# Kernel optimization log

Measured on AMD Instinct MI355X. Metric: run time of the kernel, lower is better.

Reference implementation:

```python
import jax, jax.numpy as jnp
import numpy as np

RANK = 4
ALPHA = 4.0
SCALE = ALPHA / RANK


def setup_inputs() -> dict:
    key = jax.random.key(0)
    k1, k2, k3, k4 = jax.random.split(key, 4)
    B, S, H = 4, 2048, 2048
    NH, HD = 16, 128
    x = jax.random.normal(k1, (B, S, H), dtype=jnp.float32)
    W_orig = jax.random.normal(k2, (H, NH, HD), dtype=jnp.float32) * (1.0 / np.sqrt(H))
    A_kernel = jax.random.normal(k3, (H, RANK), dtype=jnp.float32) * (1.0 / RANK)
    # B kernel is zero-init in the module; use small randn so the LoRA path is exercised
    B_kernel = jax.random.normal(k4, (RANK, NH, HD), dtype=jnp.float32) * 0.02
    return {"x": x, "W_orig": W_orig, "A_kernel": A_kernel, "B_kernel": B_kernel}


def reference(x, W_orig, A_kernel, B_kernel):
    # original layer: EinsumDense 'abc,cde->abde'  [B,S,H] x [H,NH,HD] -> [B,S,NH,HD]
    original_output = jnp.einsum('bsc,chd->bshd', x, W_orig)
    # LoRA path: Dense to rank, then EinsumDense back up, scaled
    ax = x @ A_kernel                                   # [B,S,r]
    lora_output = jnp.einsum('bsr,rhd->bshd', ax, B_kernel) * SCALE
    return original_output + lora_output
```

## Files before the change

kernel.cpp:

```cpp
#include <hip/hip_runtime.h>
#include <hip/hip_bf16.h>
#include <cstdint>


using bf16 = __hip_bfloat16;
typedef __attribute__((ext_vector_type(8))) __bf16 bf16x8;
typedef __attribute__((ext_vector_type(4))) float f32x4;

constexpr int Mdim = 8192;
constexpr int Ndim = 2048;
constexpr int Kdim = 2048;
constexpr float SCALE = 1.0f;

constexpr int BM = 256, BN = 256, BK = 64;
constexpr int NT2 = Kdim / (2 * BK);
constexpr int CVT_BLOCKS = (Mdim * Kdim) / (256 * 8);
constexpr int PREP_BLOCKS = (Ndim / 64) * (Kdim / 64);

__device__ __forceinline__ void gload_lds16(const void* g, void* l) {
  __builtin_amdgcn_global_load_lds(
      (const __attribute__((address_space(1))) uint32_t*)g,
      (__attribute__((address_space(3))) uint32_t*)l,
      16, 0, 0);
}

__global__ void prep_all(const float* __restrict__ X,
                         const float* __restrict__ W,
                         const float* __restrict__ A,
                         const float* __restrict__ Bk,
                         uint16_t* __restrict__ Xb,
                         uint16_t* __restrict__ Wt) {
  __shared__ float tile[64][65];

  if (blockIdx.x < CVT_BLOCKS) {
    const int i = blockIdx.x * blockDim.x + threadIdx.x;
    const float4* Xv = (const float4*)X;
    float4 a = Xv[i * 2 + 0];
    float4 b = Xv[i * 2 + 1];
    uint16_t o[8];
    o[0] = __bfloat16_as_ushort(__float2bfloat16(a.x));
    o[1] = __bfloat16_as_ushort(__float2bfloat16(a.y));
    o[2] = __bfloat16_as_ushort(__float2bfloat16(a.z));
    o[3] = __bfloat16_as_ushort(__float2bfloat16(a.w));
    o[4] = __bfloat16_as_ushort(__float2bfloat16(b.x));
    o[5] = __bfloat16_as_ushort(__float2bfloat16(b.y));
    o[6] = __bfloat16_as_ushort(__float2bfloat16(b.z));
    o[7] = __bfloat16_as_ushort(__float2bfloat16(b.w));
    *reinterpret_cast<uint4*>(Xb + (size_t)i * 8) = *reinterpret_cast<uint4*>(o);
  } else {
    const int pid = blockIdx.x - CVT_BLOCKS;
    const int tx = threadIdx.x & 63;
    const int ty = threadIdx.x >> 6;
    const int n0 = (pid & 31) * 64, k0 = (pid >> 5) * 64;

    const int n = n0 + tx;
    const float b0 = Bk[0 * Ndim + n];
    const float b1 = Bk[1 * Ndim + n];
    const float b2 = Bk[2 * Ndim + n];
    const float b3 = Bk[3 * Ndim + n];

    for (int i = ty; i < 64; i += 4) {
      const int k = k0 + i;
      float w = W[(size_t)k * Ndim + n];
      w += SCALE * (A[k * 4 + 0] * b0 + A[k * 4 + 1] * b1 +
                    A[k * 4 + 2] * b2 + A[k * 4 + 3] * b3);
      tile[tx][i] = w;
    }
    __syncthreads();
    for (int i = ty; i < 64; i += 4) {
      Wt[(size_t)(n0 + i) * Kdim + (k0 + tx)] =
          __bfloat16_as_ushort(__float2bfloat16(tile[i][tx]));
    }
  }
}

#define FENCE() asm volatile("" ::: "memory")
#define VMW(N)  asm volatile("s_waitcnt vmcnt(" #N ")" ::: "memory")
#define LGKM8() asm volatile("s_waitcnt lgkmcnt(8)" ::: "memory")
#define PMID()                                                                 \
  do {                                                                         \
    FENCE();                                                                   \
    __builtin_amdgcn_s_barrier();                                              \
    asm volatile("s_waitcnt lgkmcnt(0)" ::: "memory");                         \
  } while (0)
#define PEND()                                                                 \
  do {                                                                         \
    FENCE();                                                                   \
    __builtin_amdgcn_s_barrier();                                              \
    FENCE();                                                                   \
  } while (0)

__global__ __launch_bounds__(512, 2) void gemm_8ph(
    const uint16_t* __restrict__ X, const uint16_t* __restrict__ Wt,
    float* __restrict__ out) {
  __shared__ uint16_t lds[65536];

  const int t = threadIdx.x;
  const int wave = t >> 6, lane = t & 63;
  const int wm = wave >> 2, wn = wave & 3;
  const int l15 = lane & 15, kg = lane >> 4;
  const int sw = l15 & 7;

  const int lid = blockIdx.x;
  const int xcd = lid & 7, loc = lid >> 3;
  const int by = xcd * 4 + (loc & 3);
  const int bx = loc >> 2;
  const int m0 = by * BM, n0 = bx * BN;

  const uint16_t* Ag = X + (size_t)m0 * Kdim;
  const uint16_t* Bg = Wt + (size_t)n0 * Kdim;

  const int r8 = lane >> 3;
  const int gc = (lane & 7) ^ r8;
  const int slot0 = wave * 2, slot1 = slot0 + 1;
  const size_t go0 = (size_t)(slot0 * 8 + r8) * Kdim + gc * 8;
  const size_t go1 = (size_t)(slot1 * 8 + r8) * Kdim + gc * 8;

  int aE[2], bE[2];
#pragma unroll
  for (int s2 = 0; s2 < 2; ++s2) {
    const int p = (s2 * 4 + kg) ^ sw;
    aE[s2] = (wm * 64 + l15) * 64 + p * 8;
    bE[s2] = (wn * 32 + l15) * 64 + p * 8;
  }

#define STAGE_A(buf, h, kt)                                                    \
  do {                                                                         \
    gload_lds16(Ag + go0 + (size_t)(h) * 128 * Kdim + (kt),                    \
                &lds[(buf) * 32768 + (h) * 8192 + slot0 * 512]);               \
    gload_lds16(Ag + go1 + (size_t)(h) * 128 * Kdim + (kt),                    \
                &lds[(buf) * 32768 + (h) * 8192 + slot1 * 512]);               \
  } while (0)
#define STAGE_B(buf, h, kt)                                                    \
  do {                                                                         \
    gload_lds16(Bg + go0 + (size_t)(h) * 128 * Kdim + (kt),                    \
                &lds[(buf) * 32768 + 16384 + (h) * 8192 + slot0 * 512]);       \
    gload_lds16(Bg + go1 + (size_t)(h) * 128 * Kdim + (kt),                    \
                &lds[(buf) * 32768 + 16384 + (h) * 8192 + slot1 * 512]);       \
  } while (0)

  bf16x8 a[4][2], b0[2][2], b1[2][2];
  f32x4 acc[8][4] = {};

#define READ_A(QM, buf)                                                        \
  do {                                                                         \
    _Pragma("unroll") for (int ii = 0; ii < 4; ++ii)                           \
        _Pragma("unroll") for (int s2 = 0; s2 < 2; ++s2)                       \
            a[ii][s2] = *reinterpret_cast<const bf16x8*>(                      \
                &lds[(buf) * 32768 + (QM) * 8192 + ii * 1024 + aE[s2]]);       \
  } while (0)
#define READ_B(QN, buf, dst)                                                   \
  do {                                                                         \
    _Pragma("unroll") for (int jj = 0; jj < 2; ++jj)                           \
        _Pragma("unroll") for (int s2 = 0; s2 < 2; ++s2)                       \
            dst[jj][s2] = *reinterpret_cast<const bf16x8*>(                    \
                &lds[(buf) * 32768 + 16384 + (QN) * 8192 + jj * 1024 +         \
                     bE[s2]]);                                                 \
  } while (0)
#define MMA(QM, QN, barr)                                                      \
  do {                                                                         \
    __builtin_amdgcn_s_setprio(1);                                             \
    _Pragma("unroll") for (int s2 = 0; s2 < 2; ++s2)                           \
        _Pragma("unroll") for (int ii = 0; ii < 4; ++ii)                       \
            _Pragma("unroll") for (int jj = 0; jj < 2; ++jj)                   \
                acc[(QM) * 4 + ii][(QN) * 2 + jj] =                            \
                    __builtin_amdgcn_mfma_f32_16x16x32_bf16(                   \
                        a[ii][s2], barr[jj][s2],                               \
                        acc[(QM) * 4 + ii][(QN) * 2 + jj], 0, 0, 0);           \
    __builtin_amdgcn_s_setprio(0);                                             \
  } while (0)
#define STORE_Q(QM, QN)                                                        \
  do {                                                                         \
    _Pragma("unroll") for (int ii = 0; ii < 4; ++ii) {                         \
      const int mb = m0 + (QM) * 128 + wm * 64 + ii * 16 + kg * 4;             \
      _Pragma("unroll") for (int jj = 0; jj < 2; ++jj) {                       \
        const int n = n0 + (QN) * 128 + wn * 32 + jj * 16 + l15;               \
        _Pragma("unroll") for (int r = 0; r < 4; ++r)                          \
            out[(size_t)(mb + r) * Ndim + n] =                                 \
                acc[(QM) * 4 + ii][(QN) * 2 + jj][r];                          \
      }                                                                        \
    }                                                                          \
  } while (0)

  STAGE_B(0, 0, 0); STAGE_A(0, 0, 0); STAGE_B(0, 1, 0); STAGE_A(0, 1, 0);
  FENCE();
  STAGE_B(1, 0, BK); STAGE_A(1, 0, BK); STAGE_B(1, 1, BK); STAGE_A(1, 1, BK);
  FENCE();
  VMW(8);
  __builtin_amdgcn_s_barrier();
  FENCE();

#pragma unroll 1
  for (int j = 0; j < NT2 - 1; ++j) {
    const int kn0 = j * 128 + 128;
    const int kn1 = j * 128 + 192;

    READ_A(0, 0); READ_B(0, 0, b0);
    LGKM8();
    PMID(); MMA(0, 0, b0); PEND();

    READ_B(1, 0, b1);
    STAGE_B(0, 0, kn0);
    PMID(); MMA(0, 1, b1); PEND();

    READ_A(1, 0);
    STAGE_A(0, 0, kn0);
    PMID(); MMA(1, 1, b1); PEND();

    STAGE_B(0, 1, kn0); VMW(6);
    PMID(); MMA(1, 0, b0); PEND();

    READ_A(0, 1); READ_B(0, 1, b0);
    STAGE_A(0, 1, kn0);
    LGKM8();
    PMID(); MMA(0, 0, b0); PEND();

    READ_B(1, 1, b1);
    STAGE_B(1, 0, kn1);
    PMID(); MMA(0, 1, b1); PEND();

    READ_A(1, 1);
    STAGE_A(1, 0, kn1);
    PMID(); MMA(1, 1, b1); PEND();

    STAGE_B(1, 1, kn1); STAGE_A(1, 1, kn1); VMW(8);
    PMID(); MMA(1, 0, b0); PEND();
  }

  READ_A(0, 0); READ_B(0, 0, b0);
  LGKM8();
  PMID(); MMA(0, 0, b0); PEND();
  READ_B(1, 0, b1);
  PMID(); MMA(0, 1, b1); PEND();
  READ_A(1, 0);
  PMID(); MMA(1, 1, b1); PEND();
  VMW(0);
  PMID(); MMA(1, 0, b0); PEND();
  READ_A(0, 1); READ_B(0, 1, b0);
  LGKM8();
  PMID(); MMA(0, 0, b0); STORE_Q(0, 0); PEND();
  READ_B(1, 1, b1);
  PMID(); MMA(0, 1, b1); STORE_Q(0, 1); PEND();
  READ_A(1, 1);
  PMID(); MMA(1, 1, b1); STORE_Q(1, 1); PEND();
  PMID(); MMA(1, 0, b0); STORE_Q(1, 0);

#undef STAGE_A
#undef STAGE_B
#undef READ_A
#undef READ_B
#undef MMA
#undef STORE_Q
}

extern "C" void kernel_launch(void* const* d_in, const int* in_sizes, int n_in,
                              void* d_out, int out_size, void* d_ws, size_t ws_size,
                              hipStream_t stream) {
  const float* x  = (const float*)d_in[0];
  const float* W  = (const float*)d_in[1];
  const float* A  = (const float*)d_in[2];
  const float* Bk = (const float*)d_in[3];
  float* out = (float*)d_out;

  uint16_t* Xb = (uint16_t*)d_ws;
  uint16_t* Wt = (uint16_t*)((char*)d_ws + (size_t)Mdim * Kdim * 2);

  prep_all<<<CVT_BLOCKS + PREP_BLOCKS, 256, 0, stream>>>(x, W, A, Bk, Xb, Wt);

  gemm_8ph<<<(Mdim / BM) * (Ndim / BN), 512, 0, stream>>>(Xb, Wt, out);
}
```

Baseline: 190.7 us.

## Software-pipeline LDS fragment reads one phase ahead of MFMA issue

```diff
diff --git a/kernel.cpp b/kernel.cpp
--- a/kernel.cpp
+++ b/kernel.cpp
@@ -76,14 +76,7 @@
 
 #define FENCE() asm volatile("" ::: "memory")
 #define VMW(N)  asm volatile("s_waitcnt vmcnt(" #N ")" ::: "memory")
-#define LGKM8() asm volatile("s_waitcnt lgkmcnt(8)" ::: "memory")
-#define PMID()                                                                 \
-  do {                                                                         \
-    FENCE();                                                                   \
-    __builtin_amdgcn_s_barrier();                                              \
-    asm volatile("s_waitcnt lgkmcnt(0)" ::: "memory");                         \
-  } while (0)
-#define PEND()                                                                 \
+#define PH()                                                                   \
   do {                                                                         \
     FENCE();                                                                   \
     __builtin_amdgcn_s_barrier();                                              \
@@ -168,6 +161,7 @@
                         a[ii][s2], barr[jj][s2],                               \
                         acc[(QM) * 4 + ii][(QN) * 2 + jj], 0, 0, 0);           \
     __builtin_amdgcn_s_setprio(0);                                             \
+    __builtin_amdgcn_sched_barrier(0);                                         \
   } while (0)
 #define STORE_Q(QM, QN)                                                        \
   do {                                                                         \
@@ -184,66 +178,38 @@
 
   STAGE_B(0, 0, 0); STAGE_A(0, 0, 0); STAGE_B(0, 1, 0); STAGE_A(0, 1, 0);
   FENCE();
-  STAGE_B(1, 0, BK); STAGE_A(1, 0, BK); STAGE_B(1, 1, BK); STAGE_A(1, 1, BK);
+  STAGE_B(1, 0, BK); STAGE_A(1, 0, BK); STAGE_B(1, 1, BK);
   FENCE();
-  VMW(8);
-  __builtin_amdgcn_s_barrier();
-  FENCE();
+  VMW(6); PH();
+  READ_A(0, 0); READ_B(0, 0, b0);
+  STAGE_A(1, 1, BK);
 
 #pragma unroll 1
   for (int j = 0; j < NT2 - 1; ++j) {
     const int kn0 = j * 128 + 128;
     const int kn1 = j * 128 + 192;
 
-    READ_A(0, 0); READ_B(0, 0, b0);
-    LGKM8();
-    PMID(); MMA(0, 0, b0); PEND();
-
-    READ_B(1, 0, b1);
-    STAGE_B(0, 0, kn0);
-    PMID(); MMA(0, 1, b1); PEND();
-
-    READ_A(1, 0);
-    STAGE_A(0, 0, kn0);
-    PMID(); MMA(1, 1, b1); PEND();
-
-    STAGE_B(0, 1, kn0); VMW(6);
-    PMID(); MMA(1, 0, b0); PEND();
-
-    READ_A(0, 1); READ_B(0, 1, b0);
-    STAGE_A(0, 1, kn0);
-    LGKM8();
-    PMID(); MMA(0, 0, b0); PEND();
-
-    READ_B(1, 1, b1);
-    STAGE_B(1, 0, kn1);
-    PMID(); MMA(0, 1, b1); PEND();
-
-    READ_A(1, 1);
-    STAGE_A(1, 0, kn1);
-    PMID(); MMA(1, 1, b1); PEND();
-
-    STAGE_B(1, 1, kn1); STAGE_A(1, 1, kn1); VMW(8);
-    PMID(); MMA(1, 0, b0); PEND();
+    PH(); MMA(0, 0, b0); READ_B(1, 0, b1);
+    PH(); MMA(0, 1, b1); READ_A(1, 0); STAGE_B(0, 0, kn0);
+    PH(); MMA(1, 1, b1); STAGE_A(0, 0, kn0);
+    VMW(6); PH(); MMA(1, 0, b0);
+    READ_A(0, 1); READ_B(0, 1, b0); STAGE_B(0, 1, kn0);
+    PH(); MMA(0, 0, b0); READ_B(1, 1, b1); STAGE_A(0, 1, kn0);
+    VMW(8); PH(); MMA(0, 1, b1);
+    READ_A(1, 1); STAGE_B(1, 0, kn1); STAGE_A(1, 0, kn1);
+    PH(); MMA(1, 1, b1); STAGE_B(1, 1, kn1);
+    VMW(6); PH(); MMA(1, 0, b0);
+    READ_A(0, 0); READ_B(0, 0, b0); STAGE_A(1, 1, kn1);
   }
 
-  READ_A(0, 0); READ_B(0, 0, b0);
-  LGKM8();
-  PMID(); MMA(0, 0, b0); PEND();
-  READ_B(1, 0, b1);
-  PMID(); MMA(0, 1, b1); PEND();
-  READ_A(1, 0);
-  PMID(); MMA(1, 1, b1); PEND();
-  VMW(0);
-  PMID(); MMA(1, 0, b0); PEND();
-  READ_A(0, 1); READ_B(0, 1, b0);
-  LGKM8();
-  PMID(); MMA(0, 0, b0); STORE_Q(0, 0); PEND();
-  READ_B(1, 1, b1);
-  PMID(); MMA(0, 1, b1); STORE_Q(0, 1); PEND();
-  READ_A(1, 1);
-  PMID(); MMA(1, 1, b1); STORE_Q(1, 1); PEND();
-  PMID(); MMA(1, 0, b0); STORE_Q(1, 0);
+  PH(); MMA(0, 0, b0); READ_B(1, 0, b1);
+  PH(); MMA(0, 1, b1); READ_A(1, 0);
+  PH(); MMA(1, 1, b1);
+  VMW(4); PH(); MMA(1, 0, b0); READ_A(0, 1); READ_B(0, 1, b0);
+  VMW(0); PH(); MMA(0, 0, b0); READ_B(1, 1, b1); STORE_Q(0, 0);
+  PH(); MMA(0, 1, b1); READ_A(1, 1); STORE_Q(0, 1);
+  PH(); MMA(1, 1, b1); STORE_Q(1, 1);
+  PH(); MMA(1, 0, b0); STORE_Q(1, 0);
 
 #undef STAGE_A
 #undef STAGE_B
```

After: 191.2 us. No clear change (+0.2%).
